# Optimization experiments

Hardware: AMD Instinct MI355X
Metric: run time of the kernel (lower is better)

## Reference

```python
import jax, jax.numpy as jnp
import numpy as np

N = 1_000_000   # samples
D_IN = 100      # covariate dim (cfg_density[0][0])
H = 64          # hidden dim
NUM_HEADS = 5   # t-bins [0,.2,.4,.6,.8,1.0]


def setup_inputs() -> dict:
    key = jax.random.key(0)
    ks = jax.random.split(key, 17)
    s = 0.05  # param scale for numerical stability (torch init is data-independent anyway)
    return {
        "t": jax.random.uniform(ks[0], (N,), dtype=jnp.float32),
        "x": jax.random.normal(ks[1], (N, D_IN), dtype=jnp.float32),
        # density feature MLP (two Linear+ReLU layers)
        "dW1": jax.random.normal(ks[2], (D_IN, H), dtype=jnp.float32) * s,
        "db1": jax.random.normal(ks[3], (H,), dtype=jnp.float32) * s,
        "dW2": jax.random.normal(ks[4], (H, H), dtype=jnp.float32) * s,
        "db2": jax.random.normal(ks[5], (H,), dtype=jnp.float32) * s,
        # 5 multi-head branches, each 3 Treat_Linear layers (istreat=1 since isenhance=1)
        "hw1": jax.random.normal(ks[6], (NUM_HEADS, H, H), dtype=jnp.float32) * s,
        "htw1": jax.random.normal(ks[7], (NUM_HEADS, H), dtype=jnp.float32) * s,
        "hb1": jax.random.normal(ks[8], (NUM_HEADS, H), dtype=jnp.float32) * s,
        "hw2": jax.random.normal(ks[9], (NUM_HEADS, H, H), dtype=jnp.float32) * s,
        "htw2": jax.random.normal(ks[10], (NUM_HEADS, H), dtype=jnp.float32) * s,
        "hb2": jax.random.normal(ks[11], (NUM_HEADS, H), dtype=jnp.float32) * s,
        "hw3": jax.random.normal(ks[12], (NUM_HEADS, H, 1), dtype=jnp.float32) * s,
        "htw3": jax.random.normal(ks[13], (NUM_HEADS, 1), dtype=jnp.float32) * s,
        "hb3": jax.random.normal(ks[14], (NUM_HEADS, 1), dtype=jnp.float32) * s,
    }


def reference(t, x, dW1, db1, dW2, db2,
              hw1, htw1, hb1, hw2, htw2, hb2, hw3, htw3, hb3):
    # hidden_features: Linear+ReLU, Linear+ReLU
    h = jax.nn.relu(x @ dW1 + db1)        # [N, H]
    h = jax.nn.relu(h @ dW2 + db2)        # [N, H]

    tt = t[:, None]                        # treatment column [N, 1]
    # bin index per row: t in [0.2*q, 0.2*(q+1)); last bin closed at 1.0
    bins = jnp.clip(jnp.floor(t * NUM_HEADS).astype(jnp.int32), 0, NUM_HEADS - 1)

    out = jnp.zeros((x.shape[0], 1), dtype=h.dtype)
    for q in range(NUM_HEADS):  # fixed small set of structurally-distinct heads
        # Treat_Linear layer 1: feat@W + t*tw + b, relu
        a = jax.nn.relu(h @ hw1[q] + tt * htw1[q] + hb1[q])
        # Treat_Linear layer 2
        a = jax.nn.relu(a @ hw2[q] + tt * htw2[q] + hb2[q])
        # last layer: no activation, islastlayer=1
        a = a @ hw3[q] + tt * htw3[q] + hb3[q]   # [N, 1]
        out = out + jnp.where((bins == q)[:, None], a, 0.0)
    return out  # Drnet returns (None, Q); g is None so we return Q
```

## Files before the change

kernel.cpp:

```cpp
#include <hip/hip_runtime.h>

typedef _Float16 f16;
typedef _Float16 f16x8 __attribute__((ext_vector_type(8)));
typedef float f32x16 __attribute__((ext_vector_type(16)));

#define NB 5
#define DIN 100
#define NT 512
#define GRID 256
#define NWAVES (GRID * 8)

#define FID_W2 14
#define FID_HD 22
#define NFID   (FID_HD + NB * 16)
#define NENT   (NFID * 64)

__global__ __launch_bounds__(256)
void prepack_kernel(const float* __restrict__ dW1, const float* __restrict__ dW2,
                    const float* __restrict__ hw1, const float* __restrict__ hw2,
                    f16x8* __restrict__ pw)
{
    int E = blockIdx.x * 256 + threadIdx.x;
    if (E >= NENT) return;
    int lane = E & 63, fid = E >> 6;
    const float* src; int ks, mt, kmax;
    if (fid < FID_W2)      { int f = fid;          ks = f >> 1; mt = f & 1; src = dW1; kmax = 100; }
    else if (fid < FID_HD) { int f = fid - FID_W2; ks = f >> 1; mt = f & 1; src = dW2; kmax = 64; }
    else {
        int f = fid - FID_HD; int q = f >> 4; int r = f & 15;
        int layer = r >> 3; int rr = r & 7; ks = rr >> 1; mt = rr & 1;
        src = (layer ? hw2 : hw1) + q * 4096; kmax = 64;
    }
    f16x8 v;
    #pragma unroll
    for (int e = 0; e < 8; ++e) {
        int k = 16 * ks + 8 * (lane >> 5) + e;
        int m = 32 * mt + (lane & 31);
        v[e] = (k < kmax) ? (f16)src[k * 64 + m] : (f16)0.f;
    }
    pw[E] = v;
}

__device__ __forceinline__ f32x16 mfma32(f16x8 a, f16x8 b, f32x16 c) {
    return __builtin_amdgcn_mfma_f32_32x32x16_f16(a, b, c, 0, 0, 0);
}
__device__ __forceinline__ f32x16 vzero() {
    f32x16 z;
    #pragma unroll
    for (int i = 0; i < 16; ++i) z[i] = 0.f;
    return z;
}
__device__ __forceinline__ unsigned pk2(float a, float b) {
    union { f16 h[2]; unsigned u; } z; z.h[0] = (f16)a; z.h[1] = (f16)b; return z.u;
}
__device__ __forceinline__ f16x8 frag4(unsigned a, unsigned b, unsigned c, unsigned d) {
    union { unsigned u[4]; f16x8 v; } z; z.u[0]=a; z.u[1]=b; z.u[2]=c; z.u[3]=d; return z.v;
}

#define EPI8T(W, A, BIAS, TW, RT, OFF) { \
    const float4* bp_ = (const float4*)((BIAS) + (OFF)); \
    const float4* tp_ = (const float4*)((TW) + (OFF)); \
    float4 b0_=bp_[0], b1_=bp_[2], b2_=bp_[4], b3_=bp_[6]; \
    float4 t0_=tp_[0], t1_=tp_[2], t2_=tp_[4], t3_=tp_[6]; \
    W[0]=pk2(fmaxf(A[0]+b0_.x+(RT)*t0_.x,0.f), fmaxf(A[1]+b0_.y+(RT)*t0_.y,0.f)); \
    W[1]=pk2(fmaxf(A[2]+b0_.z+(RT)*t0_.z,0.f), fmaxf(A[3]+b0_.w+(RT)*t0_.w,0.f)); \
    W[2]=pk2(fmaxf(A[4]+b1_.x+(RT)*t1_.x,0.f), fmaxf(A[5]+b1_.y+(RT)*t1_.y,0.f)); \
    W[3]=pk2(fmaxf(A[6]+b1_.z+(RT)*t1_.z,0.f), fmaxf(A[7]+b1_.w+(RT)*t1_.w,0.f)); \
    W[4]=pk2(fmaxf(A[8]+b2_.x+(RT)*t2_.x,0.f), fmaxf(A[9]+b2_.y+(RT)*t2_.y,0.f)); \
    W[5]=pk2(fmaxf(A[10]+b2_.z+(RT)*t2_.z,0.f), fmaxf(A[11]+b2_.w+(RT)*t2_.w,0.f)); \
    W[6]=pk2(fmaxf(A[12]+b3_.x+(RT)*t3_.x,0.f), fmaxf(A[13]+b3_.y+(RT)*t3_.y,0.f)); \
    W[7]=pk2(fmaxf(A[14]+b3_.z+(RT)*t3_.z,0.f), fmaxf(A[15]+b3_.w+(RT)*t3_.w,0.f)); }

#define EPI8B(W, A, BIAS, OFF) { \
    const float4* bp_ = (const float4*)((BIAS) + (OFF)); \
    float4 b0_=bp_[0], b1_=bp_[2], b2_=bp_[4], b3_=bp_[6]; \
    W[0]=pk2(fmaxf(A[0]+b0_.x,0.f), fmaxf(A[1]+b0_.y,0.f)); \
    W[1]=pk2(fmaxf(A[2]+b0_.z,0.f), fmaxf(A[3]+b0_.w,0.f)); \
    W[2]=pk2(fmaxf(A[4]+b1_.x,0.f), fmaxf(A[5]+b1_.y,0.f)); \
    W[3]=pk2(fmaxf(A[6]+b1_.z,0.f), fmaxf(A[7]+b1_.w,0.f)); \
    W[4]=pk2(fmaxf(A[8]+b2_.x,0.f), fmaxf(A[9]+b2_.y,0.f)); \
    W[5]=pk2(fmaxf(A[10]+b2_.z,0.f), fmaxf(A[11]+b2_.w,0.f)); \
    W[6]=pk2(fmaxf(A[12]+b3_.x,0.f), fmaxf(A[13]+b3_.y,0.f)); \
    W[7]=pk2(fmaxf(A[14]+b3_.z,0.f), fmaxf(A[15]+b3_.w,0.f)); }

#define MKB(dst, Wm, jb) { \
    unsigned s0_=__shfl_xor(Wm[jb+0],32,64), s1_=__shfl_xor(Wm[jb+1],32,64); \
    unsigned s2_=__shfl_xor(Wm[jb+2],32,64), s3_=__shfl_xor(Wm[jb+3],32,64); \
    dst = frag4(lo ? Wm[jb+0] : s2_, lo ? Wm[jb+1] : s3_, \
                lo ? s0_ : Wm[jb+2], lo ? s1_ : Wm[jb+3]); }

#define ACC16(P, A, B2, T2, W3, RT, OFF) { \
    const float4* bb_=(const float4*)((B2)+(OFF)); const float4* tt_=(const float4*)((T2)+(OFF)); \
    const float4* ww_=(const float4*)((W3)+(OFF)); \
    float4 b0_=bb_[0],b1_=bb_[2],b2_=bb_[4],b3_=bb_[6]; \
    float4 t0_=tt_[0],t1_=tt_[2],t2_=tt_[4],t3_=tt_[6]; \
    float4 w0_=ww_[0],w1_=ww_[2],w2_=ww_[4],w3_=ww_[6]; \
    P += fmaxf(A[0]+b0_.x+(RT)*t0_.x,0.f)*w0_.x + fmaxf(A[1]+b0_.y+(RT)*t0_.y,0.f)*w0_.y \
       + fmaxf(A[2]+b0_.z+(RT)*t0_.z,0.f)*w0_.z + fmaxf(A[3]+b0_.w+(RT)*t0_.w,0.f)*w0_.w \
       + fmaxf(A[4]+b1_.x+(RT)*t1_.x,0.f)*w1_.x + fmaxf(A[5]+b1_.y+(RT)*t1_.y,0.f)*w1_.y \
       + fmaxf(A[6]+b1_.z+(RT)*t1_.z,0.f)*w1_.z + fmaxf(A[7]+b1_.w+(RT)*t1_.w,0.f)*w1_.w \
       + fmaxf(A[8]+b2_.x+(RT)*t2_.x,0.f)*w2_.x + fmaxf(A[9]+b2_.y+(RT)*t2_.y,0.f)*w2_.y \
       + fmaxf(A[10]+b2_.z+(RT)*t2_.z,0.f)*w2_.z + fmaxf(A[11]+b2_.w+(RT)*t2_.w,0.f)*w2_.w \
       + fmaxf(A[12]+b3_.x+(RT)*t3_.x,0.f)*w3_.x + fmaxf(A[13]+b3_.y+(RT)*t3_.y,0.f)*w3_.y \
       + fmaxf(A[14]+b3_.z+(RT)*t3_.z,0.f)*w3_.z + fmaxf(A[15]+b3_.w+(RT)*t3_.w,0.f)*w3_.w; }

__global__ __launch_bounds__(NT, 2)
void drnet_main(const float* __restrict__ t, const float* __restrict__ x,
                const float* __restrict__ db1, const float* __restrict__ db2,
                const float* __restrict__ hb1, const float* __restrict__ htw1,
                const float* __restrict__ hb2, const float* __restrict__ htw2,
                const float* __restrict__ hw3, const float* __restrict__ htw3,
                const float* __restrict__ hb3,
                const f16x8* __restrict__ pw,
                float* __restrict__ out, int N, int NG)
{
    __shared__ __align__(16) f16x8 swts[NENT];
    __shared__ __align__(16) float sb1f[64], sb2f[64];
    __shared__ __align__(16) float shb1[NB*64], shw1t[NB*64], shb2[NB*64], shw2t[NB*64], sw3f[NB*64];
    __shared__ float shtw3[NB], shb3[NB];
    __shared__ unsigned short ssrt[8][64];
    __shared__ float sstv[8][64];
    __shared__ float sout[8][64];

    const int tid = threadIdx.x;
    const int lane = tid & 63;
    const int wv = tid >> 6;
    const int hi = lane >> 5;
    const int sm = lane & 31;
    const bool lo = (hi == 0);

    for (int p = tid; p < 64; p += NT) { sb1f[p] = db1[p]; sb2f[p] = db2[p]; }
    for (int p = tid; p < NB*64; p += NT) {
        shb1[p] = hb1[p]; shw1t[p] = htw1[p];
        shb2[p] = hb2[p]; shw2t[p] = htw2[p];
        sw3f[p] = hw3[p];
    }
    if (tid < NB) { shtw3[tid] = htw3[tid]; shb3[tid] = hb3[tid]; }
    for (int p = tid; p < NENT; p += NT)
        ((float4*)swts)[p] = ((const float4*)pw)[p];
    __syncthreads();

    #define TF(fid) swts[(fid)*64 + lane]

    const int gw = blockIdx.x * 8 + wv;
    float tpre = t[min(gw * 64 + lane, N - 1)];

    auto do_tile = [&](const f16x8* xb, int li, int rq, float rt, int qlo, int qhiR) {
        if (qlo >= NB) return;
        const int qhi = min(qhiR, NB - 1);

        f32x16 a0 = vzero(), a1 = vzero();
        #pragma unroll
        for (int ks = 0; ks < 7; ++ks) {
            a0 = mfma32(TF(ks*2 + 0), xb[ks], a0);
            a1 = mfma32(TF(ks*2 + 1), xb[ks], a1);
        }
        unsigned WA[8], WB[8];
        EPI8B(WA, a0, sb1f, 4*hi);
        EPI8B(WB, a1, sb1f, 32 + 4*hi);
        f16x8 hb0, hb1_, hb2_, hb3_;
        MKB(hb0, WA, 0); MKB(hb1_, WA, 4); MKB(hb2_, WB, 0); MKB(hb3_, WB, 4);

        f32x16 c0 = vzero(), c1 = vzero();
        c0 = mfma32(TF(FID_W2+0), hb0, c0);  c1 = mfma32(TF(FID_W2+1), hb0, c1);
        c0 = mfma32(TF(FID_W2+2), hb1_, c0); c1 = mfma32(TF(FID_W2+3), hb1_, c1);
        c0 = mfma32(TF(FID_W2+4), hb2_, c0); c1 = mfma32(TF(FID_W2+5), hb2_, c1);
        c0 = mfma32(TF(FID_W2+6), hb3_, c0); c1 = mfma32(TF(FID_W2+7), hb3_, c1);
        unsigned UA[8], UB[8];
        EPI8B(UA, c0, sb2f, 4*hi);
        EPI8B(UB, c1, sb2f, 32 + 4*hi);
        f16x8 g0, g1, g2, g3;
        MKB(g0, UA, 0); MKB(g1, UA, 4); MKB(g2, UB, 0); MKB(g3, UB, 4);

        #pragma unroll 1
        for (int q = qlo; q <= qhi; ++q) {
            const int hf = FID_HD + q * 16;
            f32x16 d0 = vzero(), d1 = vzero();
            d0 = mfma32(TF(hf+0), g0, d0);  d1 = mfma32(TF(hf+1), g0, d1);
            d0 = mfma32(TF(hf+2), g1, d0);  d1 = mfma32(TF(hf+3), g1, d1);
            d0 = mfma32(TF(hf+4), g2, d0);  d1 = mfma32(TF(hf+5), g2, d1);
            d0 = mfma32(TF(hf+6), g3, d0);  d1 = mfma32(TF(hf+7), g3, d1);
            unsigned VA[8], VB[8];
            EPI8T(VA, d0, shb1 + q*64, shw1t + q*64, rt, 4*hi);
            EPI8T(VB, d1, shb1 + q*64, shw1t + q*64, rt, 32 + 4*hi);
            f16x8 e0, e1, e2, e3;
            MKB(e0, VA, 0); MKB(e1, VA, 4); MKB(e2, VB, 0); MKB(e3, VB, 4);

            f32x16 f0 = vzero(), f1 = vzero();
            f0 = mfma32(TF(hf+8),  e0, f0);  f1 = mfma32(TF(hf+9),  e0, f1);
            f0 = mfma32(TF(hf+10), e1, f0);  f1 = mfma32(TF(hf+11), e1, f1);
            f0 = mfma32(TF(hf+12), e2, f0);  f1 = mfma32(TF(hf+13), e2, f1);
            f0 = mfma32(TF(hf+14), e3, f0);  f1 = mfma32(TF(hf+15), e3, f1);

            float part = 0.f;
            ACC16(part, f0, shb2 + q*64, shw2t + q*64, sw3f + q*64, rt, 4*hi);
            ACC16(part, f1, shb2 + q*64, shw2t + q*64, sw3f + q*64, rt, 32 + 4*hi);
            part += __shfl_xor(part, 32, 64);
            if (lo && rq == q)
                sout[wv][li] = part + rt * shtw3[q] + shb3[q];
        }
    };

    #pragma unroll 1
    for (int g = gw; g < NG; g += NWAVES) {
        const int i0 = g * 64 + lane;
        const float tv = tpre;
        const int qme = (i0 < N) ? min((int)(tv * 5.0f), NB - 1) : NB;

        const unsigned long long lowm = (1ull << lane) - 1ull;
        int pos = 0;
        #pragma unroll
        for (int b = 0; b <= NB; ++b) {
            unsigned long long mb = __ballot(qme == b);
            int ca = __popcll(mb), cb = __popcll(mb & lowm);
            pos += (b < qme) ? ca : ((b == qme) ? cb : 0);
        }
        ssrt[wv][pos] = (unsigned short)(lane | (qme << 8));
        sstv[wv][pos] = tv;
        __asm__ volatile("s_waitcnt lgkmcnt(0)" ::: "memory");

        const unsigned short pk0 = ssrt[wv][sm];
        const unsigned short pk1 = ssrt[wv][32 + sm];
        const int li0 = pk0 & 63, rq0 = pk0 >> 8;
        const int li1 = pk1 & 63, rq1 = pk1 >> 8;
        const float rt0 = sstv[wv][sm], rt1 = sstv[wv][32 + sm];
        const int qlo0 = ssrt[wv][0]  >> 8, qh0 = ssrt[wv][31] >> 8;
        const int qlo1 = ssrt[wv][32] >> 8, qh1 = ssrt[wv][63] >> 8;

        const float4* xA = (const float4*)(x + (size_t)min(g*64 + li0, N - 1) * DIN);
        const float4* xB = (const float4*)(x + (size_t)min(g*64 + li1, N - 1) * DIN);
        float4 rA[13], rB[13];
        #pragma unroll
        for (int ks = 0; ks < 6; ++ks) { rA[2*ks] = xA[4*ks + 2*hi]; rA[2*ks+1] = xA[4*ks + 2*hi + 1]; }
        rA[12] = lo ? xA[24] : make_float4(0.f, 0.f, 0.f, 0.f);
        #pragma unroll
        for (int ks = 0; ks < 6; ++ks) { rB[2*ks] = xB[4*ks + 2*hi]; rB[2*ks+1] = xB[4*ks + 2*hi + 1]; }
        rB[12] = lo ? xB[24] : make_float4(0.f, 0.f, 0.f, 0.f);

        { int gn = g + NWAVES; tpre = (gn < NG) ? t[min(gn*64 + lane, N - 1)] : 0.f; }

        f16x8 xb[7];
        #pragma unroll
        for (int ks = 0; ks < 6; ++ks)
            xb[ks] = frag4(pk2(rA[2*ks].x, rA[2*ks].y),   pk2(rA[2*ks].z, rA[2*ks].w),
                           pk2(rA[2*ks+1].x, rA[2*ks+1].y), pk2(rA[2*ks+1].z, rA[2*ks+1].w));
        xb[6] = frag4(pk2(rA[12].x, rA[12].y), pk2(rA[12].z, rA[12].w), 0u, 0u);
        do_tile(xb, li0, rq0, rt0, qlo0, qh0);

        #pragma unroll
        for (int ks = 0; ks < 6; ++ks)
            xb[ks] = frag4(pk2(rB[2*ks].x, rB[2*ks].y),   pk2(rB[2*ks].z, rB[2*ks].w),
                           pk2(rB[2*ks+1].x, rB[2*ks+1].y), pk2(rB[2*ks+1].z, rB[2*ks+1].w));
        xb[6] = frag4(pk2(rB[12].x, rB[12].y), pk2(rB[12].z, rB[12].w), 0u, 0u);
        do_tile(xb, li1, rq1, rt1, qlo1, qh1);

        __asm__ volatile("s_waitcnt lgkmcnt(0)" ::: "memory");
        const int ig = g * 64 + lane;
        if (ig < N) out[ig] = sout[wv][lane];
    }
    #undef TF
}

extern "C" void kernel_launch(void* const* d_in, const int* in_sizes, int n_in,
                              void* d_out, int out_size, void* d_ws, size_t ws_size,
                              hipStream_t stream) {
    const float* t    = (const float*)d_in[0];
    const float* x    = (const float*)d_in[1];
    const float* dW1  = (const float*)d_in[2];
    const float* db1  = (const float*)d_in[3];
    const float* dW2  = (const float*)d_in[4];
    const float* db2  = (const float*)d_in[5];
    const float* hw1  = (const float*)d_in[6];
    const float* htw1 = (const float*)d_in[7];
    const float* hb1  = (const float*)d_in[8];
    const float* hw2  = (const float*)d_in[9];
    const float* htw2 = (const float*)d_in[10];
    const float* hb2  = (const float*)d_in[11];
    const float* hw3  = (const float*)d_in[12];
    const float* htw3 = (const float*)d_in[13];
    const float* hb3  = (const float*)d_in[14];
    float* out = (float*)d_out;

    const int N = in_sizes[0];
    const int NG = (N + 63) / 64;
    f16x8* pw = (f16x8*)d_ws;

    prepack_kernel<<<(NENT + 255) / 256, 256, 0, stream>>>(dW1, dW2, hw1, hw2, pw);
    drnet_main<<<GRID, NT, 0, stream>>>(t, x, db1, db2, hb1, htw1, hb2, htw2,
                                        hw3, htw3, hb3, pw, out, N, NG);
}
```

Baseline: 154.2 us.

## Software-pipeline x row loads across wave tile iterations

Restructures the per-wave loop so each wave's gather loads of x rows are issued one stage ahead. The second half-tile's rows are fetched before the first half-tile is computed. The next group's sort and first-half loads are issued before the current group's second half-tile is computed. The aim is to hide global-memory latency behind MFMA work, with sched_barrier keeping the compiler from reordering loads and compute. The cost is higher register pressure from two live raw buffers, which may reduce occupancy or cause spills.

```diff
diff --git a/kernel.cpp b/kernel.cpp
--- a/kernel.cpp
+++ b/kernel.cpp
@@ -142,9 +142,6 @@
 
     #define TF(fid) swts[(fid)*64 + lane]
 
-    const int gw = blockIdx.x * 8 + wv;
-    float tpre = t[min(gw * 64 + lane, N - 1)];
-
     auto do_tile = [&](const f16x8* xb, int li, int rq, float rt, int qlo, int qhiR) {
         if (qlo >= NB) return;
         const int qhi = min(qhiR, NB - 1);
@@ -201,12 +198,9 @@
         }
     };
 
-    #pragma unroll 1
-    for (int g = gw; g < NG; g += NWAVES) {
-        const int i0 = g * 64 + lane;
-        const float tv = tpre;
-        const int qme = (i0 < N) ? min((int)(tv * 5.0f), NB - 1) : NB;
-
+    auto sortw = [&](int gn, float tvn) {
+        const int i0 = gn * 64 + lane;
+        const int qme = (i0 < N) ? min((int)(tvn * 5.0f), NB - 1) : NB;
         const unsigned long long lowm = (1ull << lane) - 1ull;
         int pos = 0;
         #pragma unroll
@@ -216,43 +210,63 @@
             pos += (b < qme) ? ca : ((b == qme) ? cb : 0);
         }
         ssrt[wv][pos] = (unsigned short)(lane | (qme << 8));
-        sstv[wv][pos] = tv;
+        sstv[wv][pos] = tvn;
         __asm__ volatile("s_waitcnt lgkmcnt(0)" ::: "memory");
-
-        const unsigned short pk0 = ssrt[wv][sm];
-        const unsigned short pk1 = ssrt[wv][32 + sm];
+    };
+
+    auto issue_x = [&](float4* r, int gn, int li) {
+        const float4* xp = (const float4*)(x + (size_t)min(gn * 64 + li, N - 1) * DIN);
+        #pragma unroll
+        for (int ks = 0; ks < 6; ++ks) { r[2*ks] = xp[4*ks + 2*hi]; r[2*ks+1] = xp[4*ks + 2*hi + 1]; }
+        r[12] = lo ? xp[24] : make_float4(0.f, 0.f, 0.f, 0.f);
+    };
+
+    auto convert = [&](f16x8* xb, const float4* r) {
+        #pragma unroll
+        for (int ks = 0; ks < 6; ++ks)
+            xb[ks] = frag4(pk2(r[2*ks].x, r[2*ks].y),   pk2(r[2*ks].z, r[2*ks].w),
+                           pk2(r[2*ks+1].x, r[2*ks+1].y), pk2(r[2*ks+1].z, r[2*ks+1].w));
+        xb[6] = frag4(pk2(r[12].x, r[12].y), pk2(r[12].z, r[12].w), 0u, 0u);
+    };
+
+    const int gw = blockIdx.x * 8 + wv;
+    const int S = NWAVES;
+
+    float4 raw0[13], raw1[13];
+    float treg = 0.f;
+    int g = gw;
+    if (g < NG) {
+        treg = t[min(g * 64 + lane, N - 1)];
+        sortw(g, treg);
+        { int li = ssrt[wv][sm] & 63; issue_x(raw0, g, li); }
+        { int gn = g + S; treg = (gn < NG) ? t[min(gn * 64 + lane, N - 1)] : 0.f; }
+    }
+
+    #pragma unroll 1
+    for (; g < NG; g += S) {
+        const unsigned short pk0 = ssrt[wv][sm], pk1 = ssrt[wv][32 + sm];
         const int li0 = pk0 & 63, rq0 = pk0 >> 8;
         const int li1 = pk1 & 63, rq1 = pk1 >> 8;
         const float rt0 = sstv[wv][sm], rt1 = sstv[wv][32 + sm];
         const int qlo0 = ssrt[wv][0]  >> 8, qh0 = ssrt[wv][31] >> 8;
         const int qlo1 = ssrt[wv][32] >> 8, qh1 = ssrt[wv][63] >> 8;
 
-        const float4* xA = (const float4*)(x + (size_t)min(g*64 + li0, N - 1) * DIN);
-        const float4* xB = (const float4*)(x + (size_t)min(g*64 + li1, N - 1) * DIN);
-        float4 rA[13], rB[13];
-        #pragma unroll
-        for (int ks = 0; ks < 6; ++ks) { rA[2*ks] = xA[4*ks + 2*hi]; rA[2*ks+1] = xA[4*ks + 2*hi + 1]; }
-        rA[12] = lo ? xA[24] : make_float4(0.f, 0.f, 0.f, 0.f);
-        #pragma unroll
-        for (int ks = 0; ks < 6; ++ks) { rB[2*ks] = xB[4*ks + 2*hi]; rB[2*ks+1] = xB[4*ks + 2*hi + 1]; }
-        rB[12] = lo ? xB[24] : make_float4(0.f, 0.f, 0.f, 0.f);
-
-        { int gn = g + NWAVES; tpre = (gn < NG) ? t[min(gn*64 + lane, N - 1)] : 0.f; }
-
-        f16x8 xb[7];
-        #pragma unroll
-        for (int ks = 0; ks < 6; ++ks)
-            xb[ks] = frag4(pk2(rA[2*ks].x, rA[2*ks].y),   pk2(rA[2*ks].z, rA[2*ks].w),
-                           pk2(rA[2*ks+1].x, rA[2*ks+1].y), pk2(rA[2*ks+1].z, rA[2*ks+1].w));
-        xb[6] = frag4(pk2(rA[12].x, rA[12].y), pk2(rA[12].z, rA[12].w), 0u, 0u);
-        do_tile(xb, li0, rq0, rt0, qlo0, qh0);
-
-        #pragma unroll
-        for (int ks = 0; ks < 6; ++ks)
-            xb[ks] = frag4(pk2(rB[2*ks].x, rB[2*ks].y),   pk2(rB[2*ks].z, rB[2*ks].w),
-                           pk2(rB[2*ks+1].x, rB[2*ks+1].y), pk2(rB[2*ks+1].z, rB[2*ks+1].w));
-        xb[6] = frag4(pk2(rB[12].x, rB[12].y), pk2(rB[12].z, rB[12].w), 0u, 0u);
-        do_tile(xb, li1, rq1, rt1, qlo1, qh1);
+        issue_x(raw1, g, li1);
+        f16x8 xb0[7], xb1[7];
+        convert(xb0, raw0);
+        __builtin_amdgcn_sched_barrier(0);
+        do_tile(xb0, li0, rq0, rt0, qlo0, qh0);
+        __builtin_amdgcn_sched_barrier(0);
+
+        const bool last = (g + S >= NG);
+        if (!last) {
+            sortw(g + S, treg);
+            { int gn2 = g + 2 * S; treg = (gn2 < NG) ? t[min(gn2 * 64 + lane, N - 1)] : 0.f; }
+            { int li = ssrt[wv][sm] & 63; issue_x(raw0, g + S, li); }
+            __builtin_amdgcn_sched_barrier(0);
+        }
+        convert(xb1, raw1);
+        do_tile(xb1, li1, rq1, rt1, qlo1, qh1);
 
         __asm__ volatile("s_waitcnt lgkmcnt(0)" ::: "memory");
         const int ig = g * 64 + lane;
```

New measurement: 150.6 us. 2.4% less time.

## Stage x windows in swizzled LDS via coalesced block loads with software pipelining

Applied to the files above, without the earlier changes.

Replaces the per-wave row gathers of x with block-cooperative, coalesced float4 loads of 256-row windows. The data is converted to fp16 and stored in a swizzled LDS buffer. Loads for the next window are split into two batches and interleaved with the MFMA compute of the current window, and the t prefetch and bin sort for the next window run one step ahead. The first-layer weights move into registers, and each wave now handles half of a 64-row group. The cost is higher register and LDS pressure and extra block-wide barriers each iteration.

```diff
diff --git a/kernel.cpp b/kernel.cpp
--- a/kernel.cpp
+++ b/kernel.cpp
@@ -3,12 +3,14 @@
 typedef _Float16 f16;
 typedef _Float16 f16x8 __attribute__((ext_vector_type(8)));
 typedef float f32x16 __attribute__((ext_vector_type(16)));
+typedef unsigned long long u64;
 
 #define NB 5
 #define DIN 100
 #define NT 512
 #define GRID 256
-#define NWAVES (GRID * 8)
+#define WSZ 256
+#define WF4 (WSZ * 25)
 
 #define FID_W2 14
 #define FID_HD 22
@@ -56,6 +58,12 @@
 __device__ __forceinline__ f16x8 frag4(unsigned a, unsigned b, unsigned c, unsigned d) {
     union { unsigned u[4]; f16x8 v; } z; z.u[0]=a; z.u[1]=b; z.u[2]=c; z.u[3]=d; return z.v;
 }
+__device__ __forceinline__ u64 packf4(float4 v) {
+    union { f16 h[4]; u64 u; } z;
+    z.h[0]=(f16)v.x; z.h[1]=(f16)v.y; z.h[2]=(f16)v.z; z.h[3]=(f16)v.w;
+    return z.u;
+}
+__device__ __forceinline__ int SB(int r, int b) { return (r * 224 + b) ^ ((r & 7) << 4); }
 
 #define EPI8T(W, A, BIAS, TW, RT, OFF) { \
     const float4* bp_ = (const float4*)((BIAS) + (OFF)); \
@@ -112,153 +120,213 @@
                 const float* __restrict__ hw3, const float* __restrict__ htw3,
                 const float* __restrict__ hb3,
                 const f16x8* __restrict__ pw,
-                float* __restrict__ out, int N, int NG)
+                float* __restrict__ out, int N, int NWIN)
 {
-    __shared__ __align__(16) f16x8 swts[NENT];
+    __shared__ __align__(16) unsigned char sxs[WSZ * 224];
+    __shared__ __align__(16) f16x8 sHD[NB * 16 * 64];
+    __shared__ __align__(16) f16x8 sW2[8 * 64];
     __shared__ __align__(16) float sb1f[64], sb2f[64];
     __shared__ __align__(16) float shb1[NB*64], shw1t[NB*64], shb2[NB*64], shw2t[NB*64], sw3f[NB*64];
     __shared__ float shtw3[NB], shb3[NB];
     __shared__ unsigned short ssrt[8][64];
     __shared__ float sstv[8][64];
-    __shared__ float sout[8][64];
+    __shared__ float sout[WSZ];
 
     const int tid = threadIdx.x;
     const int lane = tid & 63;
     const int wv = tid >> 6;
+    const int p = wv >> 1;
+    const int h = wv & 1;
     const int hi = lane >> 5;
     const int sm = lane & 31;
     const bool lo = (hi == 0);
 
-    for (int p = tid; p < 64; p += NT) { sb1f[p] = db1[p]; sb2f[p] = db2[p]; }
-    for (int p = tid; p < NB*64; p += NT) {
-        shb1[p] = hb1[p]; shw1t[p] = htw1[p];
-        shb2[p] = hb2[p]; shw2t[p] = htw2[p];
-        sw3f[p] = hw3[p];
+    for (int idx = tid; idx < NB*16*64; idx += NT)
+        ((float4*)sHD)[idx] = ((const float4*)(pw + FID_HD*64))[idx];
+    for (int idx = tid; idx < 8*64; idx += NT)
+        ((float4*)sW2)[idx] = ((const float4*)(pw + FID_W2*64))[idx];
+    for (int q = tid; q < 64; q += NT) { sb1f[q] = db1[q]; sb2f[q] = db2[q]; }
+    for (int q = tid; q < NB*64; q += NT) {
+        shb1[q] = hb1[q]; shw1t[q] = htw1[q];
+        shb2[q] = hb2[q]; shw2t[q] = htw2[q];
+        sw3f[q] = hw3[q];
     }
     if (tid < NB) { shtw3[tid] = htw3[tid]; shb3[tid] = hb3[tid]; }
-    for (int p = tid; p < NENT; p += NT)
-        ((float4*)swts)[p] = ((const float4*)pw)[p];
-    __syncthreads();
-
-    #define TF(fid) swts[(fid)*64 + lane]
-
-    const int gw = blockIdx.x * 8 + wv;
-    float tpre = t[min(gw * 64 + lane, N - 1)];
-
-    auto do_tile = [&](const f16x8* xb, int li, int rq, float rt, int qlo, int qhiR) {
-        if (qlo >= NB) return;
-        const int qhi = min(qhiR, NB - 1);
-
-        f32x16 a0 = vzero(), a1 = vzero();
-        #pragma unroll
-        for (int ks = 0; ks < 7; ++ks) {
-            a0 = mfma32(TF(ks*2 + 0), xb[ks], a0);
-            a1 = mfma32(TF(ks*2 + 1), xb[ks], a1);
-        }
-        unsigned WA[8], WB[8];
-        EPI8B(WA, a0, sb1f, 4*hi);
-        EPI8B(WB, a1, sb1f, 32 + 4*hi);
-        f16x8 hb0, hb1_, hb2_, hb3_;
-        MKB(hb0, WA, 0); MKB(hb1_, WA, 4); MKB(hb2_, WB, 0); MKB(hb3_, WB, 4);
-
-        f32x16 c0 = vzero(), c1 = vzero();
-        c0 = mfma32(TF(FID_W2+0), hb0, c0);  c1 = mfma32(TF(FID_W2+1), hb0, c1);
-        c0 = mfma32(TF(FID_W2+2), hb1_, c0); c1 = mfma32(TF(FID_W2+3), hb1_, c1);
-        c0 = mfma32(TF(FID_W2+4), hb2_, c0); c1 = mfma32(TF(FID_W2+5), hb2_, c1);
-        c0 = mfma32(TF(FID_W2+6), hb3_, c0); c1 = mfma32(TF(FID_W2+7), hb3_, c1);
-        unsigned UA[8], UB[8];
-        EPI8B(UA, c0, sb2f, 4*hi);
-        EPI8B(UB, c1, sb2f, 32 + 4*hi);
-        f16x8 g0, g1, g2, g3;
-        MKB(g0, UA, 0); MKB(g1, UA, 4); MKB(g2, UB, 0); MKB(g3, UB, 4);
-
-        #pragma unroll 1
-        for (int q = qlo; q <= qhi; ++q) {
-            const int hf = FID_HD + q * 16;
-            f32x16 d0 = vzero(), d1 = vzero();
-            d0 = mfma32(TF(hf+0), g0, d0);  d1 = mfma32(TF(hf+1), g0, d1);
-            d0 = mfma32(TF(hf+2), g1, d0);  d1 = mfma32(TF(hf+3), g1, d1);
-            d0 = mfma32(TF(hf+4), g2, d0);  d1 = mfma32(TF(hf+5), g2, d1);
-            d0 = mfma32(TF(hf+6), g3, d0);  d1 = mfma32(TF(hf+7), g3, d1);
-            unsigned VA[8], VB[8];
-            EPI8T(VA, d0, shb1 + q*64, shw1t + q*64, rt, 4*hi);
-            EPI8T(VB, d1, shb1 + q*64, shw1t + q*64, rt, 32 + 4*hi);
-            f16x8 e0, e1, e2, e3;
-            MKB(e0, VA, 0); MKB(e1, VA, 4); MKB(e2, VB, 0); MKB(e3, VB, 4);
-
-            f32x16 f0 = vzero(), f1 = vzero();
-            f0 = mfma32(TF(hf+8),  e0, f0);  f1 = mfma32(TF(hf+9),  e0, f1);
-            f0 = mfma32(TF(hf+10), e1, f0);  f1 = mfma32(TF(hf+11), e1, f1);
-            f0 = mfma32(TF(hf+12), e2, f0);  f1 = mfma32(TF(hf+13), e2, f1);
-            f0 = mfma32(TF(hf+14), e3, f0);  f1 = mfma32(TF(hf+15), e3, f1);
-
-            float part = 0.f;
-            ACC16(part, f0, shb2 + q*64, shw2t + q*64, sw3f + q*64, rt, 4*hi);
-            ACC16(part, f1, shb2 + q*64, shw2t + q*64, sw3f + q*64, rt, 32 + 4*hi);
-            part += __shfl_xor(part, 32, 64);
-            if (lo && rq == q)
-                sout[wv][li] = part + rt * shtw3[q] + shb3[q];
-        }
-    };
-
-    #pragma unroll 1
-    for (int g = gw; g < NG; g += NWAVES) {
-        const int i0 = g * 64 + lane;
-        const float tv = tpre;
-        const int qme = (i0 < N) ? min((int)(tv * 5.0f), NB - 1) : NB;
-
-        const unsigned long long lowm = (1ull << lane) - 1ull;
+
+    f16x8 w1f[14];
+    #pragma unroll
+    for (int u = 0; u < 14; ++u) w1f[u] = pw[u * 64 + lane];
+
+    auto sortw = [&](int Wn, float tv) {
+        const long long i0 = (long long)Wn * WSZ + p * 64 + lane;
+        const int qme = (i0 < (long long)N) ? min((int)(tv * 5.0f), NB - 1) : NB;
+        const u64 lowm = (1ull << lane) - 1ull;
         int pos = 0;
         #pragma unroll
         for (int b = 0; b <= NB; ++b) {
-            unsigned long long mb = __ballot(qme == b);
+            u64 mb = __ballot(qme == b);
             int ca = __popcll(mb), cb = __popcll(mb & lowm);
             pos += (b < qme) ? ca : ((b == qme) ? cb : 0);
         }
         ssrt[wv][pos] = (unsigned short)(lane | (qme << 8));
         sstv[wv][pos] = tv;
         __asm__ volatile("s_waitcnt lgkmcnt(0)" ::: "memory");
-
-        const unsigned short pk0 = ssrt[wv][sm];
-        const unsigned short pk1 = ssrt[wv][32 + sm];
-        const int li0 = pk0 & 63, rq0 = pk0 >> 8;
-        const int li1 = pk1 & 63, rq1 = pk1 >> 8;
-        const float rt0 = sstv[wv][sm], rt1 = sstv[wv][32 + sm];
-        const int qlo0 = ssrt[wv][0]  >> 8, qh0 = ssrt[wv][31] >> 8;
-        const int qlo1 = ssrt[wv][32] >> 8, qh1 = ssrt[wv][63] >> 8;
-
-        const float4* xA = (const float4*)(x + (size_t)min(g*64 + li0, N - 1) * DIN);
-        const float4* xB = (const float4*)(x + (size_t)min(g*64 + li1, N - 1) * DIN);
-        float4 rA[13], rB[13];
-        #pragma unroll
-        for (int ks = 0; ks < 6; ++ks) { rA[2*ks] = xA[4*ks + 2*hi]; rA[2*ks+1] = xA[4*ks + 2*hi + 1]; }
-        rA[12] = lo ? xA[24] : make_float4(0.f, 0.f, 0.f, 0.f);
-        #pragma unroll
-        for (int ks = 0; ks < 6; ++ks) { rB[2*ks] = xB[4*ks + 2*hi]; rB[2*ks+1] = xB[4*ks + 2*hi + 1]; }
-        rB[12] = lo ? xB[24] : make_float4(0.f, 0.f, 0.f, 0.f);
-
-        { int gn = g + NWAVES; tpre = (gn < NG) ? t[min(gn*64 + lane, N - 1)] : 0.f; }
+    };
+
+    const size_t XMAX = (size_t)N * 25 - 1;
+
+    int W = blockIdx.x;
+    {
+        float t0 = t[min((size_t)W * WSZ + p * 64 + lane, (size_t)(N - 1))];
+        sortw(W, t0);
+    }
+    float tnext;
+    {
+        float4 rawP[13];
+        const size_t base4 = (size_t)W * WF4;
+        #pragma unroll
+        for (int j = 0; j < 13; ++j) {
+            int f = min(tid + NT * j, WF4 - 1);
+            rawP[j] = ((const float4*)x)[min(base4 + (size_t)f, XMAX)];
+        }
+        tnext = t[min(((size_t)W + GRID) * WSZ + p * 64 + lane, (size_t)(N - 1))];
+        #pragma unroll
+        for (int j = 0; j < 13; ++j) {
+            int f = min(tid + NT * j, WF4 - 1);
+            int row = f / 25, c4 = f % 25;
+            *(u64*)(sxs + SB(row, c4 * 8)) = packf4(rawP[j]);
+        }
+    }
+    __syncthreads();
+
+    #pragma unroll 1
+    for (; W < NWIN; W += GRID) {
+        const int WN = W + GRID;
+
+        const unsigned short pkme = ssrt[wv][h * 32 + sm];
+        const int li = pkme & 63, rq = pkme >> 8;
+        const float rt = sstv[wv][h * 32 + sm];
+        const int qlo = ssrt[wv][h * 32] >> 8;
+        const int qhi0 = ssrt[wv][h * 32 + 31] >> 8;
+        const int row = p * 64 + li;
 
         f16x8 xb[7];
         #pragma unroll
-        for (int ks = 0; ks < 6; ++ks)
-            xb[ks] = frag4(pk2(rA[2*ks].x, rA[2*ks].y),   pk2(rA[2*ks].z, rA[2*ks].w),
-                           pk2(rA[2*ks+1].x, rA[2*ks+1].y), pk2(rA[2*ks+1].z, rA[2*ks+1].w));
-        xb[6] = frag4(pk2(rA[12].x, rA[12].y), pk2(rA[12].z, rA[12].w), 0u, 0u);
-        do_tile(xb, li0, rq0, rt0, qlo0, qh0);
-
-        #pragma unroll
-        for (int ks = 0; ks < 6; ++ks)
-            xb[ks] = frag4(pk2(rB[2*ks].x, rB[2*ks].y),   pk2(rB[2*ks].z, rB[2*ks].w),
-                           pk2(rB[2*ks+1].x, rB[2*ks+1].y), pk2(rB[2*ks+1].z, rB[2*ks+1].w));
-        xb[6] = frag4(pk2(rB[12].x, rB[12].y), pk2(rB[12].z, rB[12].w), 0u, 0u);
-        do_tile(xb, li1, rq1, rt1, qlo1, qh1);
-
+        for (int ks = 0; ks < 7; ++ks)
+            xb[ks] = *(const f16x8*)(sxs + SB(row, ks * 32 + hi * 16));
+        {
+            union { f16x8 v; unsigned u[4]; } z; z.v = xb[6];
+            const unsigned m0 = lo ? 0xFFFFFFFFu : 0u;
+            z.u[0] &= m0; z.u[1] &= m0; z.u[2] = 0u; z.u[3] = 0u;
+            xb[6] = z.v;
+        }
         __asm__ volatile("s_waitcnt lgkmcnt(0)" ::: "memory");
-        const int ig = g * 64 + lane;
-        if (ig < N) out[ig] = sout[wv][lane];
-    }
-    #undef TF
+        __builtin_amdgcn_sched_barrier(0);
+
+        float4 rawA[7];
+        {
+            const size_t base4 = (size_t)WN * WF4;
+            #pragma unroll
+            for (int j = 0; j < 7; ++j) {
+                int f = min(tid + NT * j, WF4 - 1);
+                rawA[j] = ((const float4*)x)[min(base4 + (size_t)f, XMAX)];
+            }
+        }
+        __syncthreads();
+
+        sortw(WN, tnext);
+        tnext = t[min(((size_t)W + 2 * GRID) * WSZ + p * 64 + lane, (size_t)(N - 1))];
+        __builtin_amdgcn_sched_barrier(0);
+
+        f16x8 g0, g1, g2, g3;
+        if (qlo < NB) {
+            f32x16 a0 = vzero(), a1 = vzero();
+            #pragma unroll
+            for (int ks = 0; ks < 7; ++ks) {
+                a0 = mfma32(w1f[ks * 2 + 0], xb[ks], a0);
+                a1 = mfma32(w1f[ks * 2 + 1], xb[ks], a1);
+            }
+            unsigned WA[8], WB[8];
+            EPI8B(WA, a0, sb1f, 4 * hi);
+            EPI8B(WB, a1, sb1f, 32 + 4 * hi);
+            f16x8 hb0, hb1_, hb2_, hb3_;
+            MKB(hb0, WA, 0); MKB(hb1_, WA, 4); MKB(hb2_, WB, 0); MKB(hb3_, WB, 4);
+
+            f32x16 c0 = vzero(), c1 = vzero();
+            c0 = mfma32(sW2[0*64+lane], hb0, c0);  c1 = mfma32(sW2[1*64+lane], hb0, c1);
+            c0 = mfma32(sW2[2*64+lane], hb1_, c0); c1 = mfma32(sW2[3*64+lane], hb1_, c1);
+            c0 = mfma32(sW2[4*64+lane], hb2_, c0); c1 = mfma32(sW2[5*64+lane], hb2_, c1);
+            c0 = mfma32(sW2[6*64+lane], hb3_, c0); c1 = mfma32(sW2[7*64+lane], hb3_, c1);
+            unsigned UA[8], UB[8];
+            EPI8B(UA, c0, sb2f, 4 * hi);
+            EPI8B(UB, c1, sb2f, 32 + 4 * hi);
+            MKB(g0, UA, 0); MKB(g1, UA, 4); MKB(g2, UB, 0); MKB(g3, UB, 4);
+        }
+        __builtin_amdgcn_sched_barrier(0);
+
+        float4 rawB[6];
+        {
+            #pragma unroll
+            for (int j = 0; j < 7; ++j) {
+                int f = min(tid + NT * j, WF4 - 1);
+                int r2 = f / 25, c4 = f % 25;
+                *(u64*)(sxs + SB(r2, c4 * 8)) = packf4(rawA[j]);
+            }
+            const size_t base4 = (size_t)WN * WF4;
+            #pragma unroll
+            for (int j = 0; j < 6; ++j) {
+                int f = min(tid + NT * (7 + j), WF4 - 1);
+                rawB[j] = ((const float4*)x)[min(base4 + (size_t)f, XMAX)];
+            }
+        }
+        __builtin_amdgcn_sched_barrier(0);
+
+        if (qlo < NB) {
+            const int qhi = min(qhi0, NB - 1);
+            #pragma unroll 1
+            for (int q = qlo; q <= qhi; ++q) {
+                const f16x8* ph = sHD + q * 16 * 64;
+                f32x16 d0 = vzero(), d1 = vzero();
+                d0 = mfma32(ph[0*64+lane], g0, d0);  d1 = mfma32(ph[1*64+lane], g0, d1);
+                d0 = mfma32(ph[2*64+lane], g1, d0);  d1 = mfma32(ph[3*64+lane], g1, d1);
+                d0 = mfma32(ph[4*64+lane], g2, d0);  d1 = mfma32(ph[5*64+lane], g2, d1);
+                d0 = mfma32(ph[6*64+lane], g3, d0);  d1 = mfma32(ph[7*64+lane], g3, d1);
+                unsigned VA[8], VB[8];
+                EPI8T(VA, d0, shb1 + q*64, shw1t + q*64, rt, 4 * hi);
+                EPI8T(VB, d1, shb1 + q*64, shw1t + q*64, rt, 32 + 4 * hi);
+                f16x8 e0, e1, e2, e3;
+                MKB(e0, VA, 0); MKB(e1, VA, 4); MKB(e2, VB, 0); MKB(e3, VB, 4);
+
+                f32x16 f0 = vzero(), f1 = vzero();
+                f0 = mfma32(ph[8*64+lane],  e0, f0);  f1 = mfma32(ph[9*64+lane],  e0, f1);
+                f0 = mfma32(ph[10*64+lane], e1, f0);  f1 = mfma32(ph[11*64+lane], e1, f1);
+                f0 = mfma32(ph[12*64+lane], e2, f0);  f1 = mfma32(ph[13*64+lane], e2, f1);
+                f0 = mfma32(ph[14*64+lane], e3, f0);  f1 = mfma32(ph[15*64+lane], e3, f1);
+
+                float part = 0.f;
+                ACC16(part, f0, shb2 + q*64, shw2t + q*64, sw3f + q*64, rt, 4 * hi);
+                ACC16(part, f1, shb2 + q*64, shw2t + q*64, sw3f + q*64, rt, 32 + 4 * hi);
+                part += __shfl_xor(part, 32, 64);
+                if (lo && rq == q)
+                    sout[p * 64 + li] = part + rt * shtw3[q] + shb3[q];
+            }
+        }
+        __builtin_amdgcn_sched_barrier(0);
+
+        #pragma unroll
+        for (int j = 0; j < 6; ++j) {
+            int f = min(tid + NT * (7 + j), WF4 - 1);
+            int r2 = f / 25, c4 = f % 25;
+            *(u64*)(sxs + SB(r2, c4 * 8)) = packf4(rawB[j]);
+        }
+
+        __syncthreads();
+
+        if (tid < WSZ) {
+            const size_t ig = (size_t)W * WSZ + tid;
+            if (ig < (size_t)N) out[ig] = sout[tid];
+        }
+    }
 }
 
 extern "C" void kernel_launch(void* const* d_in, const int* in_sizes, int n_in,
@@ -282,10 +350,10 @@
     float* out = (float*)d_out;
 
     const int N = in_sizes[0];
-    const int NG = (N + 63) / 64;
+    const int NWIN = (N + WSZ - 1) / WSZ;
     f16x8* pw = (f16x8*)d_ws;
 
     prepack_kernel<<<(NENT + 255) / 256, 256, 0, stream>>>(dW1, dW2, hw1, hw2, pw);
     drnet_main<<<GRID, NT, 0, stream>>>(t, x, db1, db2, hb1, htw1, hb2, htw2,
-                                        hw3, htw3, hb3, pw, out, N, NG);
-}
+                                        hw3, htw3, hb3, pw, out, N, NWIN);
+}
```

After: 160.5 us. 1.04x slower.
